# Performance work log

Hardware: AMD Instinct MI355X
Metric: run time of the kernel (lower is better)

Reference implementation:

```python
import jax, jax.numpy as jnp
import numpy as np

L, H, D, T, DFF, OUT, B = 6, 12, 49, 16, 1024, 10, 8192
STD = 0.02


def setup_inputs() -> dict:
    key = jax.random.key(0)
    ks = jax.random.split(key, 24)
    n = lambda k, shape: jax.random.normal(k, shape, dtype=jnp.float32) * STD
    return {
        "x": jax.random.normal(ks[0], (B, 784), dtype=jnp.float32),
        "mask": jnp.ones((B, T), dtype=bool),  # unused by the original Attention
        # per-layer, per-head Q/K/V/out linears (weights stored as (in, out))
        "Wq": n(ks[1], (L, H, D, D)), "bq": n(ks[2], (L, H, D)),
        "Wk": n(ks[3], (L, H, D, D)), "bk": n(ks[4], (L, H, D)),
        "Wv": n(ks[5], (L, H, D, D)), "bv": n(ks[6], (L, H, D)),
        "Wo": n(ks[7], (L, H, D, D)), "bo": n(ks[8], (L, H, D)),
        # concat projection Linear(D*H, D)
        "Wcat": n(ks[9], (L, H * D, D)), "bcat": n(ks[10], (L, D)),
        # LayerNorms
        "ln1_g": jnp.ones((L, D), jnp.float32), "ln1_b": jnp.zeros((L, D), jnp.float32),
        "ln2_g": jnp.ones((L, D), jnp.float32), "ln2_b": jnp.zeros((L, D), jnp.float32),
        # FeedForward
        "W1": n(ks[11], (L, D, DFF)), "b1": n(ks[12], (L, DFF)),
        "W2": n(ks[13], (L, DFF, D)), "b2": n(ks[14], (L, D)),
        # ClassificationHead
        "Wc": n(ks[15], (D, OUT)), "bc": n(ks[16], (OUT,)),
    }


def _ln(x, g, b):
    mu = jnp.mean(x, axis=-1, keepdims=True)
    var = jnp.mean((x - mu) ** 2, axis=-1, keepdims=True)
    return (x - mu) / jnp.sqrt(var + 1e-5) * g + b


def _forward(x, Wq, bq, Wk, bk, Wv, bv, Wo, bo, Wcat, bcat,
             ln1_g, ln1_b, ln2_g, ln2_b, W1, b1, W2, b2, Wc, bc):
    bsz = x.shape[0]
    h = x.reshape(bsz, T, D)  # MakeTokens
    scale = float(1.0 / np.sqrt(D))
    for i in range(L):
        xn = _ln(h, ln1_g[i], ln1_b[i])
        # all heads batched via einsum (each head attends over full d_model)
        q = jnp.einsum('btd,hde->bhte', xn, Wq[i]) + bq[i][None, :, None, :]
        k = jnp.einsum('btd,hde->bhte', xn, Wk[i]) + bk[i][None, :, None, :]
        v = jnp.einsum('btd,hde->bhte', xn, Wv[i]) + bv[i][None, :, None, :]
        w = jax.nn.softmax(jnp.einsum('bhte,bhse->bhts', q, k) * scale, axis=-1)
        o = jnp.einsum('bhts,bhse->bhte', w, v)
        o = jnp.einsum('bhte,hef->bhtf', o, Wo[i]) + bo[i][None, :, None, :]
        cat = o.transpose(0, 2, 1, 3).reshape(bsz, T, H * D)  # concat heads
        attn = cat @ Wcat[i] + bcat[i]
        x2 = h + attn  # dropout is identity at inference
        xn2 = _ln(x2, ln2_g[i], ln2_b[i])
        ff = jax.nn.relu(xn2 @ W1[i] + b1[i]) @ W2[i] + b2[i]
        h = x2 + ff
    return h[:, 0, :] @ Wc + bc  # ClassificationHead on token 0


def reference(x, mask, Wq, bq, Wk, bk, Wv, bv, Wo, bo, Wcat, bcat,
              ln1_g, ln1_b, ln2_g, ln2_b, W1, b1, W2, b2, Wc, bc):
    # mask is accepted but unused, matching the original Attention.forward
    return _forward(x, Wq, bq, Wk, bk, Wv, bv, Wo, bo, Wcat, bcat,
                    ln1_g, ln1_b, ln2_g, ln2_b, W1, b1, W2, b2, Wc, bc)
```

## Files before the change

### kernel.cpp

```cpp
#include <hip/hip_runtime.h>
#include <hip/hip_bf16.h>

#define LYR 6
#define NH 12
#define DM 49
#define FFD 1024
#define NOUT 10
#define NB 8192
#define NWIN 240

typedef __bf16 bf16x8 __attribute__((ext_vector_type(8)));
typedef float f32x4 __attribute__((ext_vector_type(4)));
typedef unsigned int u32;
typedef u32 u32x4 __attribute__((ext_vector_type(4)));

static __device__ __forceinline__ f32x4 mfma_full(u32x4 a, u32x4 b, f32x4 c) {
  return __builtin_amdgcn_mfma_f32_16x16x32_bf16(
      __builtin_bit_cast(bf16x8, a), __builtin_bit_cast(bf16x8, b), c, 0, 0, 0);
}

static __device__ __forceinline__ f32x4 mfma_hz(u32 a0, u32 a1, u32 b0, u32 b1, f32x4 c) {
  u32x4 A = {a0, a1, 0u, 0u};
  u32x4 B = {b0, b1, 0u, 0u};
  return mfma_full(A, B, c);
}

static __device__ __forceinline__ unsigned short f2bf(float f) {
  union { float f; unsigned u; } c; c.f = f;
  unsigned r = c.u + 0x7fffu + ((c.u >> 16) & 1u);
  return (unsigned short)(r >> 16);
}

static __device__ __forceinline__ u32 pk2(float a, float b) {
  __hip_bfloat162 h2 = __float22bfloat162_rn(make_float2(a, b));
  u32 r;
  __builtin_memcpy(&r, &h2, 4);
  return r;
}

static __device__ __forceinline__ void gload16(const void* gp, void* lp) {
  __builtin_amdgcn_global_load_lds(
      (const __attribute__((address_space(1))) unsigned int*)gp,
      (__attribute__((address_space(3))) unsigned int*)lp, 16, 0, 0);
}

static __device__ __forceinline__ void decode(int idx, int& d, int& col) {
  int tile = idx >> 10, ks = (idx >> 9) & 1, lane = (idx >> 3) & 63, j = idx & 7;
  col = 16 * tile + (lane & 15);
  d = 16 * (2 * ks + (j >= 4 ? 1 : 0)) + 4 * (lane >> 4) + (j & 3);
}


__global__ void prep_qkv_frag(const float* __restrict__ Wq, const float* __restrict__ bq,
                              const float* __restrict__ Wk, const float* __restrict__ bk,
                              const float* __restrict__ Wv, const float* __restrict__ bv,
                              unsigned short* __restrict__ blob) {
  int lh = blockIdx.x, l = lh / NH, hd = lh % NH;
  unsigned short* base = blob + (size_t)(l * 20 + hd) * 16384;
  for (int idx = threadIdx.x; idx < 4096; idx += blockDim.x) {
    int d, e;
    decode(idx, d, e);
    float q = 0.f, k = 0.f, v = 0.f;
    if (e < DM) {
      if (d < DM) {
        q = Wq[(size_t)lh * 2401 + d * DM + e] * (1.f / 7.f);
        k = Wk[(size_t)lh * 2401 + d * DM + e];
        v = Wv[(size_t)lh * 2401 + d * DM + e];
      } else if (d == DM) {
        q = bq[lh * DM + e] * (1.f / 7.f);
        k = bk[lh * DM + e];
        v = bv[lh * DM + e];
      }
    }
    base[idx] = f2bf(q);
    base[4096 + idx] = f2bf(k);
    base[8192 + idx] = f2bf(v);
  }
}

__global__ void prep_comb_frag(const float* __restrict__ Wo, const float* __restrict__ bo,
                               const float* __restrict__ Wcat, const float* __restrict__ bcat,
                               unsigned short* __restrict__ blob) {
  int lh = blockIdx.x, l = lh / NH, hh = lh % NH;
  unsigned short* base = blob + (size_t)(l * 20 + hh) * 16384 + 12288;
  for (int idx = threadIdx.x; idx < 4096; idx += blockDim.x) {
    int e, f;
    decode(idx, e, f);
    float val = 0.f;
    if (f < DM) {
      if (e < DM) {
        for (int c = 0; c < DM; ++c)
          val += Wo[(size_t)lh * 2401 + e * DM + c] *
                 Wcat[((size_t)l * 588 + hh * DM + c) * DM + f];
      } else if (e == DM) {
        for (int c = 0; c < DM; ++c)
          val += bo[lh * DM + c] * Wcat[((size_t)l * 588 + hh * DM + c) * DM + f];
        if (hh == 0) val += bcat[l * DM + f];
      }
    }
    base[idx] = f2bf(val);
  }
}

__global__ void prep_ff_frag(const float* __restrict__ W1, const float* __restrict__ b1,
                             const float* __restrict__ W2,
                             unsigned short* __restrict__ blob) {
  int l = blockIdx.x >> 3, part = blockIdx.x & 7;
  for (int idx = part * 16384 + threadIdx.x; idx < (part + 1) * 16384; idx += blockDim.x) {
    int c = idx >> 13, within = idx & 8191, sec = within >> 12, sidx = within & 4095;
    int fb = c >> 1, c_rel = c & 1;
    unsigned short* dst =
        blob + (size_t)(l * 20 + 12 + fb) * 16384 + c_rel * 8192 + sec * 4096;
    int d, col;
    decode(sidx, d, col);
    float v = 0.f;
    if (sec == 0) {
      int jcol = 64 * c + col;
      if (d < DM) v = W1[(size_t)l * DM * FFD + d * FFD + jcol];
      else if (d == DM) v = b1[l * FFD + jcol];
    } else {
      int jg = 64 * c + d;
      if (col < DM) v = W2[(size_t)l * FFD * DM + jg * DM + col];
    }
    dst[sidx] = f2bf(v);
  }
}

__global__ void prep_small(const float* __restrict__ g1, const float* __restrict__ b1,
                           const float* __restrict__ g2, const float* __restrict__ b2,
                           const float* __restrict__ bff2,
                           float* __restrict__ g1p, float* __restrict__ b1p,
                           float* __restrict__ g2p, float* __restrict__ b2p,
                           float* __restrict__ bff2p) {
  int idx = threadIdx.x;
  if (idx >= 384) return;
  int l = idx >> 6, d = idx & 63;
  bool v = d < DM;
  g1p[idx] = v ? g1[l * DM + d] : 0.f;
  b1p[idx] = v ? b1[l * DM + d] : 0.f;
  g2p[idx] = v ? g2[l * DM + d] : 0.f;
  b2p[idx] = v ? b2[l * DM + d] : 0.f;
  bff2p[idx] = v ? bff2[l * DM + d] : 0.f;
}


static __device__ __forceinline__ void ln_pack(const f32x4 (&h)[4], const f32x4 (&gv)[4],
                                               const f32x4 (&bv)[4], int g, u32x4 (&xf)[2]) {
  float s = 0.f, s2 = 0.f;
#pragma unroll
  for (int mi = 0; mi < 4; ++mi)
#pragma unroll
    for (int r = 0; r < 4; ++r) { float v = h[mi][r]; s += v; s2 += v * v; }
  s += __shfl_xor(s, 16, 64); s += __shfl_xor(s, 32, 64);
  s2 += __shfl_xor(s2, 16, 64); s2 += __shfl_xor(s2, 32, 64);
  float mu = s * (1.f / 49.f);
  float rs = rsqrtf(s2 * (1.f / 49.f) - mu * mu + 1e-5f);
  u32 t[8];
#pragma unroll
  for (int mi = 0; mi < 4; ++mi) {
    float xv[4];
#pragma unroll
    for (int r = 0; r < 4; ++r) xv[r] = (h[mi][r] - mu) * rs * gv[mi][r] + bv[mi][r];
    if (mi == 3) xv[1] = (g == 0) ? 1.0f : xv[1];
    t[2 * mi] = pk2(xv[0], xv[1]);
    t[2 * mi + 1] = pk2(xv[2], xv[3]);
  }
  xf[0] = u32x4{t[0], t[1], t[2], t[3]};
  xf[1] = u32x4{t[4], t[5], t[6], t[7]};
}

static __device__ __forceinline__ void softmax_pk(f32x4 s, u32& p0, u32& p1) {
  float e0 = __expf(s[0]), e1 = __expf(s[1]);
  float e2 = __expf(s[2]), e3 = __expf(s[3]);
  float su = e0 + e1 + e2 + e3;
  su += __shfl_xor(su, 16, 64);
  su += __shfl_xor(su, 32, 64);
  float inv = 1.f / su;
  p0 = pk2(e0 * inv, e1 * inv);
  p1 = pk2(e2 * inv, e3 * inv);
}

#define STAGE_LOAD(s)                                                         \
  do {                                                                        \
    const unsigned short* gsrc = blob + (size_t)(s) * 8192 + tid * 8;         \
    unsigned short* ldst = &wbuf[(s) & 1][wv * 512];                          \
    _Pragma("unroll") for (int r = 0; r < 8; ++r)                             \
        gload16(gsrc + r * 1024, ldst + r * 1024);                            \
  } while (0)

__global__ __launch_bounds__(128, 2) void transformer_kernel(
    const float* __restrict__ x, float* __restrict__ out,
    const unsigned short* __restrict__ blob,
    const float* __restrict__ lg1, const float* __restrict__ lb1,
    const float* __restrict__ lg2, const float* __restrict__ lb2,
    const float* __restrict__ b2p, const float* __restrict__ Wc,
    const float* __restrict__ bc) {
  __shared__ __align__(16) unsigned short wbuf[2][8192];
  const int tid = threadIdx.x;
  const int wv = tid >> 6, lane = tid & 63;
  const int g = lane >> 4, li = lane & 15;
  const int s0 = blockIdx.x * 8 + wv * 4;
  const f32x4 z4 = {0.f, 0.f, 0.f, 0.f};

  STAGE_LOAD(0);

  f32x4 h[4][4];
#pragma unroll
  for (int s = 0; s < 4; ++s) {
    const float* xa = x + (size_t)(s0 + s) * 784 + li * DM;
#pragma unroll
    for (int mi = 0; mi < 4; ++mi)
#pragma unroll
      for (int r = 0; r < 4; ++r) {
        int d = 16 * mi + 4 * g + r;
        h[s][mi][r] = (d < DM) ? xa[d] : 0.f;
      }
  }

  int w = 0;
  for (int layer = 0; layer < LYR; ++layer) {
    u32x4 xf[4][2];
    {
      f32x4 gv[4], bv[4];
#pragma unroll
      for (int mi = 0; mi < 4; ++mi) {
        int off = layer * 64 + 16 * mi + 4 * g;
        gv[mi] = *(const f32x4*)(lg1 + off);
        bv[mi] = *(const f32x4*)(lb1 + off);
      }
#pragma unroll
      for (int s = 0; s < 4; ++s) ln_pack(h[s], gv, bv, g, xf[s]);
    }

    for (int hd = 0; hd < NH; ++hd) {
      __syncthreads();
      if (w + 1 < NWIN) STAGE_LOAD(w + 1);
      u32 p[4][2];
      {
        const u32x4* QW = (const u32x4*)wbuf[w & 1];
        const u32x4* KW = (const u32x4*)(wbuf[w & 1] + 4096);
        u32x4 qf[4][2], kf[4][2];
        __builtin_amdgcn_s_setprio(1);
#pragma unroll
        for (int mi = 0; mi < 4; ++mi) {
          f32x4 cq[4];
#pragma unroll
          for (int s = 0; s < 4; ++s) cq[s] = z4;
#pragma unroll
          for (int ks = 0; ks < 2; ++ks) {
            u32x4 wq = QW[(mi * 2 + ks) * 64 + lane];
#pragma unroll
            for (int s = 0; s < 4; ++s) cq[s] = mfma_full(wq, xf[s][ks], cq[s]);
          }
#pragma unroll
          for (int s = 0; s < 4; ++s) {
            qf[s][mi >> 1][2 * (mi & 1)] = pk2(cq[s][0], cq[s][1]);
            qf[s][mi >> 1][2 * (mi & 1) + 1] = pk2(cq[s][2], cq[s][3]);
          }
        }
#pragma unroll
        for (int mi = 0; mi < 4; ++mi) {
          f32x4 ck[4];
#pragma unroll
          for (int s = 0; s < 4; ++s) ck[s] = z4;
#pragma unroll
          for (int ks = 0; ks < 2; ++ks) {
            u32x4 wk = KW[(mi * 2 + ks) * 64 + lane];
#pragma unroll
            for (int s = 0; s < 4; ++s) ck[s] = mfma_full(wk, xf[s][ks], ck[s]);
          }
#pragma unroll
          for (int s = 0; s < 4; ++s) {
            kf[s][mi >> 1][2 * (mi & 1)] = pk2(ck[s][0], ck[s][1]);
            kf[s][mi >> 1][2 * (mi & 1) + 1] = pk2(ck[s][2], ck[s][3]);
          }
        }
        f32x4 sc[4];
#pragma unroll
        for (int s = 0; s < 4; ++s) {
          sc[s] = mfma_full(kf[s][0], qf[s][0], z4);
          sc[s] = mfma_full(kf[s][1], qf[s][1], sc[s]);
        }
        __builtin_amdgcn_s_setprio(0);
#pragma unroll
        for (int s = 0; s < 4; ++s) softmax_pk(sc[s], p[s][0], p[s][1]);
      }
      ++w;

      __syncthreads();
      if (w + 1 < NWIN) STAGE_LOAD(w + 1);
      {
        const u32x4* VW = (const u32x4*)wbuf[w & 1];
        const u32x4* CW = (const u32x4*)(wbuf[w & 1] + 4096);
        __builtin_amdgcn_s_setprio(1);
        u32 vf_[4][4][2];
#pragma unroll
        for (int nt = 0; nt < 4; ++nt) {
          f32x4 cv[4];
#pragma unroll
          for (int s = 0; s < 4; ++s) cv[s] = z4;
#pragma unroll
          for (int ks = 0; ks < 2; ++ks) {
            u32x4 wvv = VW[(nt * 2 + ks) * 64 + lane];
#pragma unroll
            for (int s = 0; s < 4; ++s) cv[s] = mfma_full(xf[s][ks], wvv, cv[s]);
          }
#pragma unroll
          for (int s = 0; s < 4; ++s) {
            vf_[s][nt][0] = pk2(cv[s][0], cv[s][1]);
            vf_[s][nt][1] = pk2(cv[s][2], cv[s][3]);
          }
        }
        u32x4 of_[4][2];
#pragma unroll
        for (int nt = 0; nt < 4; ++nt) {
#pragma unroll
          for (int s = 0; s < 4; ++s) {
            f32x4 c = mfma_hz(vf_[s][nt][0], vf_[s][nt][1], p[s][0], p[s][1], z4);
            if (nt == 3) c[1] = (g == 0) ? 1.0f : c[1];
            of_[s][nt >> 1][2 * (nt & 1)] = pk2(c[0], c[1]);
            of_[s][nt >> 1][2 * (nt & 1) + 1] = pk2(c[2], c[3]);
          }
        }
#pragma unroll
        for (int ft = 0; ft < 4; ++ft) {
#pragma unroll
          for (int ks = 0; ks < 2; ++ks) {
            u32x4 wc = CW[(ft * 2 + ks) * 64 + lane];
#pragma unroll
            for (int s = 0; s < 4; ++s) h[s][ft] = mfma_full(wc, of_[s][ks], h[s][ft]);
          }
        }
        __builtin_amdgcn_s_setprio(0);
      }
      ++w;
    }

    {
      f32x4 gv[4], bv[4];
#pragma unroll
      for (int mi = 0; mi < 4; ++mi) {
        int off = layer * 64 + 16 * mi + 4 * g;
        gv[mi] = *(const f32x4*)(lg2 + off);
        bv[mi] = *(const f32x4*)(lb2 + off);
      }
#pragma unroll
      for (int s = 0; s < 4; ++s) ln_pack(h[s], gv, bv, g, xf[s]);
#pragma unroll
      for (int mi = 0; mi < 4; ++mi) {
        f32x4 bb = *(const f32x4*)(b2p + layer * 64 + 16 * mi + 4 * g);
#pragma unroll
        for (int s = 0; s < 4; ++s) h[s][mi] += bb;
      }
    }

    for (int c = 0; c < 16; ++c) {
      __syncthreads();
      if (w + 1 < NWIN) STAGE_LOAD(w + 1);
      const u32x4* W1c = (const u32x4*)wbuf[w & 1];
      const u32x4* W2c = (const u32x4*)(wbuf[w & 1] + 4096);
      __builtin_amdgcn_s_setprio(1);
      u32x4 af[4][2];
#pragma unroll
      for (int jt = 0; jt < 4; ++jt) {
        f32x4 ca[4];
#pragma unroll
        for (int s = 0; s < 4; ++s) ca[s] = z4;
#pragma unroll
        for (int ks = 0; ks < 2; ++ks) {
          u32x4 ww = W1c[(jt * 2 + ks) * 64 + lane];
#pragma unroll
          for (int s = 0; s < 4; ++s) ca[s] = mfma_full(ww, xf[s][ks], ca[s]);
        }
#pragma unroll
        for (int s = 0; s < 4; ++s) {
          float r0 = fmaxf(ca[s][0], 0.f), r1 = fmaxf(ca[s][1], 0.f);
          float r2 = fmaxf(ca[s][2], 0.f), r3 = fmaxf(ca[s][3], 0.f);
          af[s][jt >> 1][2 * (jt & 1)] = pk2(r0, r1);
          af[s][jt >> 1][2 * (jt & 1) + 1] = pk2(r2, r3);
        }
      }
#pragma unroll
      for (int ft = 0; ft < 4; ++ft) {
#pragma unroll
        for (int ks = 0; ks < 2; ++ks) {
          u32x4 ww = W2c[(ft * 2 + ks) * 64 + lane];
#pragma unroll
          for (int s = 0; s < 4; ++s) h[s][ft] = mfma_full(ww, af[s][ks], h[s][ft]);
        }
      }
      __builtin_amdgcn_s_setprio(0);
      ++w;
    }
  }

  __syncthreads();
  float* hs = (float*)&wbuf[0][0];
  if (li == 0) {
#pragma unroll
    for (int s = 0; s < 4; ++s)
#pragma unroll
      for (int mi = 0; mi < 4; ++mi)
#pragma unroll
        for (int r = 0; r < 4; ++r)
          hs[(wv * 4 + s) * 64 + 16 * mi + 4 * g + r] = h[s][mi][r];
  }
  __syncthreads();
  if (lane < 40) {
    int smp = lane / 10, c = lane % 10;
    float acc = bc[c];
    const float* hrow = hs + (wv * 4 + smp) * 64;
    for (int d = 0; d < DM; ++d) acc += hrow[d] * Wc[d * NOUT + c];
    out[(size_t)(s0 + smp) * NOUT + c] = acc;
  }
}

extern "C" void kernel_launch(void* const* d_in, const int* in_sizes, int n_in,
                              void* d_out, int out_size, void* d_ws, size_t ws_size,
                              hipStream_t stream) {
  const float* x = (const float*)d_in[0];
  const float* Wq = (const float*)d_in[2];
  const float* bq = (const float*)d_in[3];
  const float* Wk = (const float*)d_in[4];
  const float* bk = (const float*)d_in[5];
  const float* Wv = (const float*)d_in[6];
  const float* bv = (const float*)d_in[7];
  const float* Wo = (const float*)d_in[8];
  const float* bo = (const float*)d_in[9];
  const float* Wcat = (const float*)d_in[10];
  const float* bcat = (const float*)d_in[11];
  const float* ln1_g = (const float*)d_in[12];
  const float* ln1_b = (const float*)d_in[13];
  const float* ln2_g = (const float*)d_in[14];
  const float* ln2_b = (const float*)d_in[15];
  const float* W1 = (const float*)d_in[16];
  const float* b1 = (const float*)d_in[17];
  const float* W2 = (const float*)d_in[18];
  const float* b2 = (const float*)d_in[19];
  const float* Wc = (const float*)d_in[20];
  const float* bc = (const float*)d_in[21];

  unsigned short* blob = (unsigned short*)d_ws;
  float* fp = (float*)(blob + (size_t)NWIN * 8192);
  float* g1p = fp;
  float* b1p = g1p + 384;
  float* g2p = b1p + 384;
  float* b2lp = g2p + 384;
  float* b2p = b2lp + 384;

  prep_qkv_frag<<<72, 256, 0, stream>>>(Wq, bq, Wk, bk, Wv, bv, blob);
  prep_comb_frag<<<72, 256, 0, stream>>>(Wo, bo, Wcat, bcat, blob);
  prep_ff_frag<<<48, 256, 0, stream>>>(W1, b1, W2, blob);
  prep_small<<<1, 384, 0, stream>>>(ln1_g, ln1_b, ln2_g, ln2_b, b2, g1p, b1p, g2p, b2lp, b2p);

  transformer_kernel<<<NB / 8, 128, 0, stream>>>(
      x, (float*)d_out, blob, g1p, b1p, g2p, b2lp, b2p, Wc, bc);
}
```

Before: 612.7 us.

## Process three samples per wave, raise occupancy, use exp2 softmax

Reduces samples per wave from 4 to 3 and raises launch bounds from 2 to 3 blocks per SM, trading less weight reuse per LDS stage for more waves in flight to hide latency. The block count grows and bounds checks handle the ragged final block. The softmax scale now folds log2(e) into the Q weights so exp2f can replace __expf. Softmax is also deferred until after the V projection to shorten live ranges.

```diff
diff --git a/kernel.cpp b/kernel.cpp
--- a/kernel.cpp
+++ b/kernel.cpp
@@ -8,6 +8,7 @@
 #define NOUT 10
 #define NB 8192
 #define NWIN 240
+#define SPW 3
 
 typedef __bf16 bf16x8 __attribute__((ext_vector_type(8)));
 typedef float f32x4 __attribute__((ext_vector_type(4)));
@@ -55,6 +56,7 @@
                               const float* __restrict__ Wk, const float* __restrict__ bk,
                               const float* __restrict__ Wv, const float* __restrict__ bv,
                               unsigned short* __restrict__ blob) {
+  const float QS = 1.44269504088896f / 7.0f;
   int lh = blockIdx.x, l = lh / NH, hd = lh % NH;
   unsigned short* base = blob + (size_t)(l * 20 + hd) * 16384;
   for (int idx = threadIdx.x; idx < 4096; idx += blockDim.x) {
@@ -63,11 +65,11 @@
     float q = 0.f, k = 0.f, v = 0.f;
     if (e < DM) {
       if (d < DM) {
-        q = Wq[(size_t)lh * 2401 + d * DM + e] * (1.f / 7.f);
+        q = Wq[(size_t)lh * 2401 + d * DM + e] * QS;
         k = Wk[(size_t)lh * 2401 + d * DM + e];
         v = Wv[(size_t)lh * 2401 + d * DM + e];
       } else if (d == DM) {
-        q = bq[lh * DM + e] * (1.f / 7.f);
+        q = bq[lh * DM + e] * QS;
         k = bk[lh * DM + e];
         v = bv[lh * DM + e];
       }
@@ -170,8 +172,8 @@
 }
 
 static __device__ __forceinline__ void softmax_pk(f32x4 s, u32& p0, u32& p1) {
-  float e0 = __expf(s[0]), e1 = __expf(s[1]);
-  float e2 = __expf(s[2]), e3 = __expf(s[3]);
+  float e0 = exp2f(s[0]), e1 = exp2f(s[1]);
+  float e2 = exp2f(s[2]), e3 = exp2f(s[3]);
   float su = e0 + e1 + e2 + e3;
   su += __shfl_xor(su, 16, 64);
   su += __shfl_xor(su, 32, 64);
@@ -188,7 +190,7 @@
         gload16(gsrc + r * 1024, ldst + r * 1024);                            \
   } while (0)
 
-__global__ __launch_bounds__(128, 2) void transformer_kernel(
+__global__ __launch_bounds__(128, 3) void transformer_kernel(
     const float* __restrict__ x, float* __restrict__ out,
     const unsigned short* __restrict__ blob,
     const float* __restrict__ lg1, const float* __restrict__ lb1,
@@ -199,15 +201,16 @@
   const int tid = threadIdx.x;
   const int wv = tid >> 6, lane = tid & 63;
   const int g = lane >> 4, li = lane & 15;
-  const int s0 = blockIdx.x * 8 + wv * 4;
+  const int s0 = (blockIdx.x * 2 + wv) * SPW;
   const f32x4 z4 = {0.f, 0.f, 0.f, 0.f};
 
   STAGE_LOAD(0);
 
-  f32x4 h[4][4];
-#pragma unroll
-  for (int s = 0; s < 4; ++s) {
-    const float* xa = x + (size_t)(s0 + s) * 784 + li * DM;
+  f32x4 h[SPW][4];
+#pragma unroll
+  for (int s = 0; s < SPW; ++s) {
+    int si = s0 + s; si = si < NB ? si : NB - 1;
+    const float* xa = x + (size_t)si * 784 + li * DM;
 #pragma unroll
     for (int mi = 0; mi < 4; ++mi)
 #pragma unroll
@@ -219,7 +222,7 @@
 
   int w = 0;
   for (int layer = 0; layer < LYR; ++layer) {
-    u32x4 xf[4][2];
+    u32x4 xf[SPW][2];
     {
       f32x4 gv[4], bv[4];
 #pragma unroll
@@ -229,61 +232,58 @@
         bv[mi] = *(const f32x4*)(lb1 + off);
       }
 #pragma unroll
-      for (int s = 0; s < 4; ++s) ln_pack(h[s], gv, bv, g, xf[s]);
+      for (int s = 0; s < SPW; ++s) ln_pack(h[s], gv, bv, g, xf[s]);
     }
 
     for (int hd = 0; hd < NH; ++hd) {
       __syncthreads();
       if (w + 1 < NWIN) STAGE_LOAD(w + 1);
-      u32 p[4][2];
+      f32x4 sc[SPW];
       {
         const u32x4* QW = (const u32x4*)wbuf[w & 1];
         const u32x4* KW = (const u32x4*)(wbuf[w & 1] + 4096);
-        u32x4 qf[4][2], kf[4][2];
+        u32x4 qf[SPW][2], kf[SPW][2];
         __builtin_amdgcn_s_setprio(1);
 #pragma unroll
         for (int mi = 0; mi < 4; ++mi) {
-          f32x4 cq[4];
-#pragma unroll
-          for (int s = 0; s < 4; ++s) cq[s] = z4;
+          f32x4 cq[SPW];
+#pragma unroll
+          for (int s = 0; s < SPW; ++s) cq[s] = z4;
 #pragma unroll
           for (int ks = 0; ks < 2; ++ks) {
             u32x4 wq = QW[(mi * 2 + ks) * 64 + lane];
 #pragma unroll
-            for (int s = 0; s < 4; ++s) cq[s] = mfma_full(wq, xf[s][ks], cq[s]);
-          }
-#pragma unroll
-          for (int s = 0; s < 4; ++s) {
+            for (int s = 0; s < SPW; ++s) cq[s] = mfma_full(wq, xf[s][ks], cq[s]);
+          }
+#pragma unroll
+          for (int s = 0; s < SPW; ++s) {
             qf[s][mi >> 1][2 * (mi & 1)] = pk2(cq[s][0], cq[s][1]);
             qf[s][mi >> 1][2 * (mi & 1) + 1] = pk2(cq[s][2], cq[s][3]);
           }
         }
 #pragma unroll
         for (int mi = 0; mi < 4; ++mi) {
-          f32x4 ck[4];
-#pragma unroll
-          for (int s = 0; s < 4; ++s) ck[s] = z4;
+          f32x4 ck[SPW];
+#pragma unroll
+          for (int s = 0; s < SPW; ++s) ck[s] = z4;
 #pragma unroll
           for (int ks = 0; ks < 2; ++ks) {
             u32x4 wk = KW[(mi * 2 + ks) * 64 + lane];
 #pragma unroll
-            for (int s = 0; s < 4; ++s) ck[s] = mfma_full(wk, xf[s][ks], ck[s]);
-          }
-#pragma unroll
-          for (int s = 0; s < 4; ++s) {
+            for (int s = 0; s < SPW; ++s) ck[s] = mfma_full(wk, xf[s][ks], ck[s]);
+          }
+#pragma unroll
+          for (int s = 0; s < SPW; ++s) {
             kf[s][mi >> 1][2 * (mi & 1)] = pk2(ck[s][0], ck[s][1]);
             kf[s][mi >> 1][2 * (mi & 1) + 1] = pk2(ck[s][2], ck[s][3]);
           }
         }
-        f32x4 sc[4];
-#pragma unroll
-        for (int s = 0; s < 4; ++s) {
+#pragma unroll
+        for (int s = 0; s < SPW; ++s) {
           sc[s] = mfma_full(kf[s][0], qf[s][0], z4);
           sc[s] = mfma_full(kf[s][1], qf[s][1], sc[s]);
         }
         __builtin_amdgcn_s_setprio(0);
-#pragma unroll
-        for (int s = 0; s < 4; ++s) softmax_pk(sc[s], p[s][0], p[s][1]);
       }
       ++w;
 
@@ -293,29 +293,32 @@
         const u32x4* VW = (const u32x4*)wbuf[w & 1];
         const u32x4* CW = (const u32x4*)(wbuf[w & 1] + 4096);
         __builtin_amdgcn_s_setprio(1);
-        u32 vf_[4][4][2];
+        u32 vf_[SPW][4][2];
 #pragma unroll
         for (int nt = 0; nt < 4; ++nt) {
-          f32x4 cv[4];
-#pragma unroll
-          for (int s = 0; s < 4; ++s) cv[s] = z4;
+          f32x4 cv[SPW];
+#pragma unroll
+          for (int s = 0; s < SPW; ++s) cv[s] = z4;
 #pragma unroll
           for (int ks = 0; ks < 2; ++ks) {
             u32x4 wvv = VW[(nt * 2 + ks) * 64 + lane];
 #pragma unroll
-            for (int s = 0; s < 4; ++s) cv[s] = mfma_full(xf[s][ks], wvv, cv[s]);
-          }
-#pragma unroll
-          for (int s = 0; s < 4; ++s) {
+            for (int s = 0; s < SPW; ++s) cv[s] = mfma_full(xf[s][ks], wvv, cv[s]);
+          }
+#pragma unroll
+          for (int s = 0; s < SPW; ++s) {
             vf_[s][nt][0] = pk2(cv[s][0], cv[s][1]);
             vf_[s][nt][1] = pk2(cv[s][2], cv[s][3]);
           }
         }
-        u32x4 of_[4][2];
+        u32 p[SPW][2];
+#pragma unroll
+        for (int s = 0; s < SPW; ++s) softmax_pk(sc[s], p[s][0], p[s][1]);
+        u32x4 of_[SPW][2];
 #pragma unroll
         for (int nt = 0; nt < 4; ++nt) {
 #pragma unroll
-          for (int s = 0; s < 4; ++s) {
+          for (int s = 0; s < SPW; ++s) {
             f32x4 c = mfma_hz(vf_[s][nt][0], vf_[s][nt][1], p[s][0], p[s][1], z4);
             if (nt == 3) c[1] = (g == 0) ? 1.0f : c[1];
             of_[s][nt >> 1][2 * (nt & 1)] = pk2(c[0], c[1]);
@@ -328,7 +331,7 @@
           for (int ks = 0; ks < 2; ++ks) {
             u32x4 wc = CW[(ft * 2 + ks) * 64 + lane];
 #pragma unroll
-            for (int s = 0; s < 4; ++s) h[s][ft] = mfma_full(wc, of_[s][ks], h[s][ft]);
+            for (int s = 0; s < SPW; ++s) h[s][ft] = mfma_full(wc, of_[s][ks], h[s][ft]);
           }
         }
         __builtin_amdgcn_s_setprio(0);
@@ -345,12 +348,12 @@
         bv[mi] = *(const f32x4*)(lb2 + off);
       }
 #pragma unroll
-      for (int s = 0; s < 4; ++s) ln_pack(h[s], gv, bv, g, xf[s]);
+      for (int s = 0; s < SPW; ++s) ln_pack(h[s], gv, bv, g, xf[s]);
 #pragma unroll
       for (int mi = 0; mi < 4; ++mi) {
         f32x4 bb = *(const f32x4*)(b2p + layer * 64 + 16 * mi + 4 * g);
 #pragma unroll
-        for (int s = 0; s < 4; ++s) h[s][mi] += bb;
+        for (int s = 0; s < SPW; ++s) h[s][mi] += bb;
       }
     }
 
@@ -360,20 +363,20 @@
       const u32x4* W1c = (const u32x4*)wbuf[w & 1];
       const u32x4* W2c = (const u32x4*)(wbuf[w & 1] + 4096);
       __builtin_amdgcn_s_setprio(1);
-      u32x4 af[4][2];
+      u32x4 af[SPW][2];
 #pragma unroll
       for (int jt = 0; jt < 4; ++jt) {
-        f32x4 ca[4];
-#pragma unroll
-        for (int s = 0; s < 4; ++s) ca[s] = z4;
+        f32x4 ca[SPW];
+#pragma unroll
+        for (int s = 0; s < SPW; ++s) ca[s] = z4;
 #pragma unroll
         for (int ks = 0; ks < 2; ++ks) {
           u32x4 ww = W1c[(jt * 2 + ks) * 64 + lane];
 #pragma unroll
-          for (int s = 0; s < 4; ++s) ca[s] = mfma_full(ww, xf[s][ks], ca[s]);
-        }
-#pragma unroll
-        for (int s = 0; s < 4; ++s) {
+          for (int s = 0; s < SPW; ++s) ca[s] = mfma_full(ww, xf[s][ks], ca[s]);
+        }
+#pragma unroll
+        for (int s = 0; s < SPW; ++s) {
           float r0 = fmaxf(ca[s][0], 0.f), r1 = fmaxf(ca[s][1], 0.f);
           float r2 = fmaxf(ca[s][2], 0.f), r3 = fmaxf(ca[s][3], 0.f);
           af[s][jt >> 1][2 * (jt & 1)] = pk2(r0, r1);
@@ -386,7 +389,7 @@
         for (int ks = 0; ks < 2; ++ks) {
           u32x4 ww = W2c[(ft * 2 + ks) * 64 + lane];
 #pragma unroll
-          for (int s = 0; s < 4; ++s) h[s][ft] = mfma_full(ww, af[s][ks], h[s][ft]);
+          for (int s = 0; s < SPW; ++s) h[s][ft] = mfma_full(ww, af[s][ks], h[s][ft]);
         }
       }
       __builtin_amdgcn_s_setprio(0);
@@ -398,20 +401,22 @@
   float* hs = (float*)&wbuf[0][0];
   if (li == 0) {
 #pragma unroll
-    for (int s = 0; s < 4; ++s)
+    for (int s = 0; s < SPW; ++s)
 #pragma unroll
       for (int mi = 0; mi < 4; ++mi)
 #pragma unroll
         for (int r = 0; r < 4; ++r)
-          hs[(wv * 4 + s) * 64 + 16 * mi + 4 * g + r] = h[s][mi][r];
+          hs[(wv * SPW + s) * 64 + 16 * mi + 4 * g + r] = h[s][mi][r];
   }
   __syncthreads();
-  if (lane < 40) {
+  if (lane < 10 * SPW) {
     int smp = lane / 10, c = lane % 10;
-    float acc = bc[c];
-    const float* hrow = hs + (wv * 4 + smp) * 64;
-    for (int d = 0; d < DM; ++d) acc += hrow[d] * Wc[d * NOUT + c];
-    out[(size_t)(s0 + smp) * NOUT + c] = acc;
+    if (s0 + smp < NB) {
+      float acc = bc[c];
+      const float* hrow = hs + (wv * SPW + smp) * 64;
+      for (int d = 0; d < DM; ++d) acc += hrow[d] * Wc[d * NOUT + c];
+      out[(size_t)(s0 + smp) * NOUT + c] = acc;
+    }
   }
 }
 
@@ -453,6 +458,7 @@
   prep_ff_frag<<<48, 256, 0, stream>>>(W1, b1, W2, blob);
   prep_small<<<1, 384, 0, stream>>>(ln1_g, ln1_b, ln2_g, ln2_b, b2, g1p, b1p, g2p, b2lp, b2p);
 
-  transformer_kernel<<<NB / 8, 128, 0, stream>>>(
+  const int nblk = (NB + 2 * SPW - 1) / (2 * SPW);
+  transformer_kernel<<<nblk, 128, 0, stream>>>(
       x, (float*)d_out, blob, g1p, b1p, g2p, b2lp, b2p, Wc, bc);
 }
```

Result: slower. 933.7 us (+52.4%).
